# Optimization experiments

Measured on AMD Instinct MI355X. Metric: run time of the kernel, lower is better.

The kernel has to match this reference:

```python
import jax, jax.numpy as jnp
import numpy as np
import math

D_MODEL = 1024
NHEAD = 16
D_K = D_MODEL // NHEAD
LAMDA_ATT = 1.0
B, L = 2, 2048


def setup_inputs() -> dict:
    key = jax.random.key(0)
    ks = jax.random.split(key, 10)
    s = 1.0 / math.sqrt(D_MODEL)
    x = jax.random.normal(ks[0], (B, L, D_MODEL), dtype=jnp.float32)
    delta_r = jax.random.uniform(ks[1], (B, L), dtype=jnp.float32)  # positive, fed to log
    Wq = jax.random.normal(ks[2], (D_MODEL, D_MODEL), dtype=jnp.float32) * s
    Wk = jax.random.normal(ks[3], (D_MODEL, D_MODEL), dtype=jnp.float32) * s
    Wv = jax.random.normal(ks[4], (D_MODEL, D_MODEL), dtype=jnp.float32) * s
    Wo = jax.random.normal(ks[5], (D_MODEL, D_MODEL), dtype=jnp.float32) * s
    bq = jnp.zeros((D_MODEL,), jnp.float32)
    bk = jnp.zeros((D_MODEL,), jnp.float32)
    bv = jnp.zeros((D_MODEL,), jnp.float32)
    bo = jnp.zeros((D_MODEL,), jnp.float32)
    return {"x": x, "delta_r": delta_r, "Wq": Wq, "bq": bq, "Wk": Wk, "bk": bk,
            "Wv": Wv, "bv": bv, "Wo": Wo, "bo": bo}


def reference(x, delta_r, Wq, bq, Wk, bk, Wv, bv, Wo, bo):
    b, l, d = x.shape
    h, dk = NHEAD, D_K

    def proj(y, W, bias):
        # [B,L,D] -> [B,H,L,dk]
        return (y @ W + bias).reshape(b, l, h, dk).transpose(0, 2, 1, 3)

    v_scaled = x * delta_r[..., None]
    q = proj(x, Wq, bq)
    k = proj(x, Wk, bk)
    v = proj(v_scaled, Wv, bv)

    scores = jnp.einsum('bhqd,bhkd->bhqk', q, k) / math.sqrt(dk)
    pos = jnp.arange(l)
    dist = jnp.abs(pos[None, :] - pos[:, None]).astype(scores.dtype)  # [L,L]
    rel_bias = LAMDA_ATT * jnp.log(delta_r + 1e-6)  # [B,L]
    scores = scores - dist[None, None] * 0.1 + rel_bias[:, None, None, :]

    attn = jax.nn.softmax(scores, axis=-1)  # dropout is identity in eval mode
    context = jnp.einsum('bhqk,bhkd->bqhd', attn, v).reshape(b, l, d)
    out = context @ Wo + bo
    return out, attn.mean(axis=1)
```

## Files before the change

kernel.cpp:

```cpp
#include <hip/hip_runtime.h>
#include <math.h>

#define DMODEL 1024
#define NHEAD  16
#define DK     64
#define BB     2
#define LL     2048
#define MTOT   (BB*LL)

#define LOG2E      1.4426950408889634f
#define SCQ        (0.125f * LOG2E)
#define C2LOG      (0.1f * LOG2E)
#define SKIP_BOUND (-24.0f)

typedef __bf16 bf16_t;
typedef __bf16 bf16x8 __attribute__((ext_vector_type(8)));
typedef __bf16 bf16x4 __attribute__((ext_vector_type(4)));
typedef float  f32x4  __attribute__((ext_vector_type(4)));

static __device__ __forceinline__ f32x4 mfma16(bf16x8 a, bf16x8 b, f32x4 c) {
    return __builtin_amdgcn_mfma_f32_16x16x32_bf16(a, b, c, 0, 0, 0);
}
static __device__ __forceinline__ float exp2f_fast(float x) {
    return __builtin_amdgcn_exp2f(x);
}
static __device__ __forceinline__ float log2f_fast(float x) {
    return __builtin_amdgcn_logf(x);
}
static __device__ __forceinline__ void gl_lds16(const bf16_t* g, bf16_t* l) {
    __builtin_amdgcn_global_load_lds(
        (const __attribute__((address_space(1))) unsigned int*)g,
        (__attribute__((address_space(3))) unsigned int*)l, 16, 0, 0);
}

__global__ __launch_bounds__(256) void prep_x_k(
    const float* __restrict__ x, const float* __restrict__ dr,
    bf16_t* __restrict__ xb, float* __restrict__ logd2)
{
    size_t gid = (size_t)blockIdx.x * 256 + threadIdx.x;
    size_t off = gid * 8;
    float4 a = *(const float4*)(x + off);
    float4 c = *(const float4*)(x + off + 4);
    float va[8] = {a.x, a.y, a.z, a.w, c.x, c.y, c.z, c.w};
    bf16x8 o1;
#pragma unroll
    for (int j = 0; j < 8; ++j) o1[j] = (bf16_t)va[j];
    *(bf16x8*)(xb + off) = o1;
    if (gid < MTOT) logd2[gid] = log2f_fast(dr[gid] + 1e-6f);
}

__global__ __launch_bounds__(256) void prep_w_k(
    const float* __restrict__ Wq, const float* __restrict__ Wk,
    const float* __restrict__ Wv, const float* __restrict__ Wo,
    bf16_t* __restrict__ Wcat, bf16_t* __restrict__ Wot)
{
    __shared__ __align__(16) float Ts[64][68];
    const int z = blockIdx.z;
    const float* W = (z == 0) ? Wq : (z == 1) ? Wk : (z == 2) ? Wv : Wo;
    bf16_t* dst = (z < 3) ? (Wcat + (size_t)z * DMODEL * DMODEL) : Wot;
    const int tid = threadIdx.x;
    const int k0 = blockIdx.x * 64, n0 = blockIdx.y * 64;
#pragma unroll
    for (int i = 0; i < 4; ++i) {
        int u = tid + 256 * i, r = u >> 4, c4 = (u & 15) * 4;
        *(float4*)&Ts[r][c4] = *(const float4*)(W + (size_t)(k0 + r) * DMODEL + n0 + c4);
    }
    __syncthreads();
#pragma unroll
    for (int i = 0; i < 2; ++i) {
        int u = tid + 256 * i, n = u >> 3, k8 = (u & 7) * 8;
        bf16x8 v;
#pragma unroll
        for (int j = 0; j < 8; ++j) v[j] = (bf16_t)Ts[k8 + j][n];
        *(bf16x8*)(dst + (size_t)(n0 + n) * DMODEL + k0 + k8) = v;
    }
}

__global__ __launch_bounds__(256, 3) void gemm128_k(
    const bf16_t* __restrict__ A, const bf16_t* __restrict__ Bt,
    const float* __restrict__ b0, const float* __restrict__ b1,
    const float* __restrict__ b2, const float* __restrict__ delta,
    float* __restrict__ outf, bf16_t* __restrict__ outQ,
    bf16_t* __restrict__ outK, bf16_t* __restrict__ outVt, int mode)
{
    __shared__ __align__(16) bf16_t Asw[128 * 64];
    __shared__ __align__(16) bf16_t Bsw[128 * 64];
    const int tid = threadIdx.x, lane = tid & 63, w = tid >> 6;
    const int quad = lane >> 4, n16 = lane & 15;
    const int wm = (w & 1) * 64, wn = (w >> 1) * 64;
    const int m0 = blockIdx.y * 128, n0 = blockIdx.x * 128;
    const int srow = lane >> 3;
    const int scb  = (lane & 7) ^ srow;

    f32x4 acc[4][4] = {};

    for (int K0 = 0; K0 < DMODEL; K0 += 64) {
        __syncthreads();
#pragma unroll
        for (int i = 0; i < 4; ++i) {
            int rb = w * 32 + i * 8;
            gl_lds16(A  + (size_t)(m0 + rb + srow) * DMODEL + K0 + scb * 8,
                     &Asw[rb * 64]);
            gl_lds16(Bt + (size_t)(n0 + rb + srow) * DMODEL + K0 + scb * 8,
                     &Bsw[rb * 64]);
        }
        __syncthreads();
#pragma unroll
        for (int kc = 0; kc < 2; ++kc) {
            const int pcb = ((kc * 4 + quad) ^ (n16 & 7)) * 8;
            bf16x8 af[4], bfv[4];
#pragma unroll
            for (int mi = 0; mi < 4; ++mi)
                af[mi] = *(const bf16x8*)&Asw[(wm + mi * 16 + n16) * 64 + pcb];
#pragma unroll
            for (int ni = 0; ni < 4; ++ni)
                bfv[ni] = *(const bf16x8*)&Bsw[(wn + ni * 16 + n16) * 64 + pcb];
#pragma unroll
            for (int mi = 0; mi < 4; ++mi)
#pragma unroll
                for (int ni = 0; ni < 4; ++ni)
                    acc[mi][ni] = mfma16(af[mi], bfv[ni], acc[mi][ni]);
        }
    }

    if (mode == 0) {
        const int region = n0 >> 10;
        if (region == 2) {
#pragma unroll
            for (int mi = 0; mi < 4; ++mi) {
                const int mbase = m0 + wm + mi * 16 + quad * 4;
                const int bidx = mbase >> 11, l = mbase & (LL - 1);
                const f32x4 dm4 = *(const f32x4*)(delta + mbase);
#pragma unroll
                for (int ni = 0; ni < 4; ++ni) {
                    const int nl = (n0 & 1023) + wn + ni * 16 + n16;
                    const int h = nl >> 6, dd = nl & 63;
                    const float bv = b2[nl];
                    bf16x4 pk;
#pragma unroll
                    for (int r = 0; r < 4; ++r)
                        pk[r] = (bf16_t)(acc[mi][ni][r] * dm4[r] + bv);
                    *(bf16x4*)(outVt + ((size_t)(bidx * NHEAD + h) * DK + dd) * LL + l) = pk;
                }
            }
        } else {
            const float* bias = (region == 0) ? b0 : b1;
            bf16_t* dst = (region == 0) ? outQ : outK;
            const float qs = (region == 0) ? SCQ : 1.0f;
#pragma unroll
            for (int mi = 0; mi < 4; ++mi) {
#pragma unroll
                for (int r = 0; r < 4; ++r) {
                    const int m = m0 + wm + mi * 16 + quad * 4 + r;
                    const int bidx = m >> 11, l = m & (LL - 1);
#pragma unroll
                    for (int ni = 0; ni < 4; ++ni) {
                        const int nl = (n0 & 1023) + wn + ni * 16 + n16;
                        const int h = nl >> 6, dd = nl & 63;
                        float v = (acc[mi][ni][r] + bias[nl]) * qs;
                        dst[(((size_t)(bidx * NHEAD + h) * LL) + l) * DK + dd] = (bf16_t)v;
                    }
                }
            }
        }
    } else {
#pragma unroll
        for (int mi = 0; mi < 4; ++mi) {
#pragma unroll
            for (int r = 0; r < 4; ++r) {
                const int m = m0 + wm + mi * 16 + quad * 4 + r;
#pragma unroll
                for (int ni = 0; ni < 4; ++ni) {
                    const int n = n0 + wn + ni * 16 + n16;
                    outf[(size_t)m * DMODEL + n] = acc[mi][ni][r] + b0[n];
                }
            }
        }
    }
}

__global__ __launch_bounds__(256, 4) void gemm_out_k(
    const bf16_t* __restrict__ A, const bf16_t* __restrict__ Bt,
    const float* __restrict__ b0, float* __restrict__ outf)
{
    __shared__ __align__(16) bf16_t Asw[64 * 64];
    __shared__ __align__(16) bf16_t Bsw[128 * 64];
    const int tid = threadIdx.x, lane = tid & 63, w = tid >> 6;
    const int quad = lane >> 4, n16 = lane & 15;
    const int wm = (w & 1) * 32, wn = (w >> 1) * 64;
    const int m0 = blockIdx.y * 64, n0 = blockIdx.x * 128;
    const int srow = lane >> 3;
    const int scb  = (lane & 7) ^ srow;

    f32x4 acc[2][4] = {};

    for (int K0 = 0; K0 < DMODEL; K0 += 64) {
        __syncthreads();
#pragma unroll
        for (int i = 0; i < 2; ++i) {
            int rb = w * 16 + i * 8;
            gl_lds16(A + (size_t)(m0 + rb + srow) * DMODEL + K0 + scb * 8,
                     &Asw[rb * 64]);
        }
#pragma unroll
        for (int i = 0; i < 4; ++i) {
            int rb = w * 32 + i * 8;
            gl_lds16(Bt + (size_t)(n0 + rb + srow) * DMODEL + K0 + scb * 8,
                     &Bsw[rb * 64]);
        }
        __syncthreads();
#pragma unroll
        for (int kc = 0; kc < 2; ++kc) {
            const int pcb = ((kc * 4 + quad) ^ (n16 & 7)) * 8;
            bf16x8 af[2], bfv[4];
#pragma unroll
            for (int mi = 0; mi < 2; ++mi)
                af[mi] = *(const bf16x8*)&Asw[(wm + mi * 16 + n16) * 64 + pcb];
#pragma unroll
            for (int ni = 0; ni < 4; ++ni)
                bfv[ni] = *(const bf16x8*)&Bsw[(wn + ni * 16 + n16) * 64 + pcb];
#pragma unroll
            for (int mi = 0; mi < 2; ++mi)
#pragma unroll
                for (int ni = 0; ni < 4; ++ni)
                    acc[mi][ni] = mfma16(af[mi], bfv[ni], acc[mi][ni]);
        }
    }
#pragma unroll
    for (int mi = 0; mi < 2; ++mi) {
#pragma unroll
        for (int r = 0; r < 4; ++r) {
            const int m = m0 + wm + mi * 16 + quad * 4 + r;
#pragma unroll
            for (int ni = 0; ni < 4; ++ni) {
                const int n = n0 + wn + ni * 16 + n16;
                outf[(size_t)m * DMODEL + n] = acc[mi][ni][r] + b0[n];
            }
        }
    }
}

__global__ __launch_bounds__(256) void stats_k(
    const bf16_t* __restrict__ Q, const bf16_t* __restrict__ K,
    const float* __restrict__ logd2, float* __restrict__ Qn,
    float* __restrict__ Kn, float* __restrict__ dlb, float* __restrict__ ldx)
{
    __shared__ float qn_s[2048], kn_s[2048], dg_s[2048];
    const int tid = threadIdx.x, bh = blockIdx.x, b = bh >> 4;
    const size_t base = (size_t)bh * LL * DK;
#pragma unroll
    for (int i = 0; i < 8; ++i) {
        const int row = tid + 256 * i;
        float qn2 = 0.f, kn2 = 0.f, dg = 0.f;
#pragma unroll
        for (int j = 0; j < 8; ++j) {
            bf16x8 qv = *(const bf16x8*)(Q + base + (size_t)row * DK + j * 8);
            bf16x8 kv = *(const bf16x8*)(K + base + (size_t)row * DK + j * 8);
#pragma unroll
            for (int e = 0; e < 8; ++e) {
                float fq = (float)qv[e], fk = (float)kv[e];
                qn2 += fq * fq; kn2 += fk * fk; dg += fq * fk;
            }
        }
        qn_s[row] = qn2;
        kn_s[row] = kn2;
        dg_s[row] = dg + logd2[b * LL + row];
    }
    __syncthreads();
    if (tid < 16) {
        float mq = 0.f, md = 1e30f;
        for (int r = 0; r < 128; ++r) {
            mq = fmaxf(mq, qn_s[tid * 128 + r]);
            md = fminf(md, dg_s[tid * 128 + r]);
        }
        Qn[bh * 16 + tid] = sqrtf(mq);
        dlb[bh * 16 + tid] = md;
    } else if (tid >= 64 && tid < 96) {
        const int t = tid - 64;
        float mk = 0.f;
        for (int r = 0; r < 64; ++r) mk = fmaxf(mk, kn_s[t * 64 + r]);
        Kn[bh * 32 + t] = sqrtf(mk);
    } else if (tid >= 128 && tid < 160 && (bh & 15) == 0) {
        const int t = tid - 128;
        float ml = -1e30f;
        for (int r = 0; r < 64; ++r) ml = fmaxf(ml, logd2[b * LL + t * 64 + r]);
        ldx[b * 32 + t] = ml;
    }
}

__global__ __launch_bounds__(256) void mlstat_k(
    const float* __restrict__ mlws, float* __restrict__ mlmin)
{
    __shared__ float s[2048];
    const int tid = threadIdx.x, bh = blockIdx.x;
#pragma unroll
    for (int i = 0; i < 8; ++i)
        s[tid + 256 * i] = mlws[(size_t)bh * LL + tid + 256 * i];
    __syncthreads();
    if (tid < 16) {
        float m = 1e30f;
        for (int r = 0; r < 128; ++r) m = fminf(m, s[tid * 128 + r]);
        mlmin[bh * 16 + tid] = m;
    }
}

__global__ __launch_bounds__(256, 4) void attn_flash_mfma_k(
    const bf16_t* __restrict__ Q, const bf16_t* __restrict__ K,
    const bf16_t* __restrict__ Vt, const float* __restrict__ logd2,
    const float* __restrict__ Qn, const float* __restrict__ Kn,
    const float* __restrict__ dlb, const float* __restrict__ ldx,
    bf16_t* __restrict__ ctx, float* __restrict__ mlout)
{
    __shared__ __align__(16) bf16_t Ks[64][72];
    __shared__ __align__(16) bf16_t Vts[64][72];
    __shared__ __align__(16) bf16_t Ps[4][16][72];
    __shared__ float logds[64];

    const int tid = threadIdx.x;
    const int lane = tid & 63, w = tid >> 6;
    const int quad = lane >> 4, n16 = lane & 15;
    const int bh = blockIdx.x, b = bh >> 4, h = bh & 15;
    const int qt = blockIdx.y, q0 = qt * 64;
    const size_t base = (size_t)bh * LL * DK;
    const int q = q0 + w * 16 + n16;

    bf16x8 qa[2];
#pragma unroll
    for (int kc = 0; kc < 2; ++kc)
        qa[kc] = *(const bf16x8*)(Q + base + (size_t)q * DK + kc * 32 + quad * 8);

    unsigned mask = 0;
    {
        const float qn = Qn[bh * 16 + (qt >> 1)], dl = dlb[bh * 16 + (qt >> 1)];
        for (int t = 0; t < 32; ++t) {
            const int kc0 = t * 64;
            const int dmin = (kc0 > q0 + 63) ? (kc0 - (q0 + 63))
                           : ((q0 > kc0 + 63) ? (q0 - (kc0 + 63)) : 0);
            const float bound = qn * Kn[bh * 32 + t] + ldx[b * 32 + t]
                              - C2LOG * (float)dmin - dl;
            if (bound > SKIP_BOUND) mask |= (1u << t);
        }
    }

    const int strow = tid >> 3, stc8 = (tid & 7) * 8;
    bf16x8 kr0, kr1, vr0, vr1;
    float ldr = 0.f;
    auto prefetch = [&](int k0) {
        kr0 = *(const bf16x8*)(K + base + (size_t)(k0 + strow) * DK + stc8);
        kr1 = *(const bf16x8*)(K + base + (size_t)(k0 + 32 + strow) * DK + stc8);
        vr0 = *(const bf16x8*)(Vt + base + (size_t)strow * LL + k0 + stc8);
        vr1 = *(const bf16x8*)(Vt + base + (size_t)(32 + strow) * LL + k0 + stc8);
        if (tid < 64) ldr = logd2[b * LL + k0 + tid];
    };

    float m_c = -1e30f, l_c = 0.f;
    f32x4 o[4] = {};
    const float dfq = (float)(q - quad * 4);

    int t = (int)__builtin_ctz(mask);
    prefetch(t * 64);
    for (;;) {
        const unsigned rem = (t < 31) ? (mask >> (t + 1)) : 0u;
        const int tn = rem ? (t + 1 + (int)__builtin_ctz(rem)) : -1;
        __syncthreads();
        *(bf16x8*)&Ks[strow][stc8]       = kr0;
        *(bf16x8*)&Ks[32 + strow][stc8]  = kr1;
        *(bf16x8*)&Vts[strow][stc8]      = vr0;
        *(bf16x8*)&Vts[32 + strow][stc8] = vr1;
        if (tid < 64) logds[tid] = ldr;
        __syncthreads();
        if (tn >= 0) prefetch(tn * 64);
        const int k0 = t * 64;

        f32x4 s[4] = {};
#pragma unroll
        for (int kc = 0; kc < 2; ++kc) {
#pragma unroll
            for (int kt = 0; kt < 4; ++kt) {
                bf16x8 kb = *(const bf16x8*)&Ks[kt * 16 + n16][kc * 32 + quad * 8];
                s[kt] = mfma16(kb, qa[kc], s[kt]);
            }
        }
        const float df = dfq - (float)k0;
#pragma unroll
        for (int kt = 0; kt < 4; ++kt) {
            f32x4 ldv = *(const f32x4*)&logds[kt * 16 + quad * 4];
#pragma unroll
            for (int r = 0; r < 4; ++r)
                s[kt][r] += ldv[r] - C2LOG * fabsf(df - (float)(kt * 16 + r));
        }
        f32x4 mx;
#pragma unroll
        for (int r = 0; r < 4; ++r)
            mx[r] = fmaxf(fmaxf(s[0][r], s[1][r]), fmaxf(s[2][r], s[3][r]));
        float rm = fmaxf(fmaxf(mx[0], mx[1]), fmaxf(mx[2], mx[3]));
        rm = fmaxf(rm, __shfl_xor(rm, 16));
        rm = fmaxf(rm, __shfl_xor(rm, 32));
        const float mn = fmaxf(m_c, rm);
        const float alpha = exp2f_fast(m_c - mn);
        if (__any(mn > m_c)) {
#pragma unroll
            for (int dt = 0; dt < 4; ++dt)
#pragma unroll
                for (int r = 0; r < 4; ++r) o[dt][r] *= alpha;
        }
        f32x4 ps = {0.f, 0.f, 0.f, 0.f};
#pragma unroll
        for (int kt = 0; kt < 4; ++kt)
#pragma unroll
            for (int r = 0; r < 4; ++r) {
                float p = exp2f_fast(s[kt][r] - mn);
                s[kt][r] = p;
                ps[r] += p;
            }
        float psum = (ps[0] + ps[1]) + (ps[2] + ps[3]);
        psum += __shfl_xor(psum, 16);
        psum += __shfl_xor(psum, 32);
        l_c = l_c * alpha + psum;
        m_c = mn;
#pragma unroll
        for (int kt = 0; kt < 4; ++kt) {
            bf16x4 pk;
#pragma unroll
            for (int r = 0; r < 4; ++r) pk[r] = (bf16_t)s[kt][r];
            *(bf16x4*)&Ps[w][n16][kt * 16 + quad * 4] = pk;
        }
        __threadfence_block();
#pragma unroll
        for (int kc = 0; kc < 2; ++kc) {
            bf16x8 pa = *(const bf16x8*)&Ps[w][n16][kc * 32 + quad * 8];
#pragma unroll
            for (int dt = 0; dt < 4; ++dt) {
                bf16x8 vb = *(const bf16x8*)&Vts[dt * 16 + n16][kc * 32 + quad * 8];
                o[dt] = mfma16(vb, pa, o[dt]);
            }
        }
        if (tn < 0) break;
        t = tn;
    }
    const float inv = 1.f / l_c;
#pragma unroll
    for (int dt = 0; dt < 4; ++dt) {
        bf16x4 ov;
#pragma unroll
        for (int r = 0; r < 4; ++r) ov[r] = (bf16_t)(o[dt][r] * inv);
        *(bf16x4*)(ctx + ((size_t)b * LL + q) * DMODEL + h * DK +
                   dt * 16 + quad * 4) = ov;
    }
    if (quad == 0)
        mlout[(size_t)bh * LL + q] = m_c + log2f_fast(l_c);
}

__global__ __launch_bounds__(256, 3) void attn_mean_mfma_k(
    const bf16_t* __restrict__ Q, const bf16_t* __restrict__ K,
    const float* __restrict__ logd2, const float* __restrict__ mlws,
    const float* __restrict__ Qn, const float* __restrict__ Kn,
    const float* __restrict__ mlmin, const float* __restrict__ ldx,
    float* __restrict__ outmean)
{
    __shared__ __align__(16) bf16_t Ks[2][64][72];
    __shared__ float mls[2][128];
    __shared__ float logds[64];

    const int tid = threadIdx.x;
    const int lane = tid & 63, w = tid >> 6;
    const int quad = lane >> 4, n16 = lane & 15;
    const int k0 = blockIdx.x * 64, q0 = blockIdx.y * 128, b = blockIdx.z;
    const int qq[2] = {q0 + w * 32 + n16, q0 + w * 32 + 16 + n16};

    if (tid < 64) logds[tid] = logd2[b * LL + k0 + tid];
    __syncthreads();

    float bias0[2][4][4];
#pragma unroll
    for (int qg = 0; qg < 2; ++qg) {
        const float df = (float)(qq[qg] - k0 - quad * 4);
#pragma unroll
        for (int kt = 0; kt < 4; ++kt) {
            f32x4 ldv = *(const f32x4*)&logds[kt * 16 + quad * 4];
#pragma unroll
            for (int r = 0; r < 4; ++r)
                bias0[qg][kt][r] = ldv[r] - C2LOG * fabsf(df - (float)(kt * 16 + r));
        }
    }

    const int qt = q0 >> 7, ktl = k0 >> 6;
    const int dmin = (k0 > q0 + 127) ? (k0 - (q0 + 127))
                   : ((q0 > k0 + 63) ? (q0 - (k0 + 63)) : 0);
    unsigned hmask = 0;
    {
        const float dterm = ldx[b * 32 + ktl] - C2LOG * (float)dmin;
        for (int h = 0; h < NHEAD; ++h) {
            const int bh = b * 16 + h;
            const float bound = Qn[bh * 16 + qt] * Kn[bh * 32 + ktl] + dterm
                              - mlmin[bh * 16 + qt];
            if (bound > SKIP_BOUND) hmask |= (1u << h);
        }
    }

    f32x4 acc[2][4] = {};

    if (hmask) {
        const int strow = tid >> 3, stc8 = (tid & 7) * 8;
        bf16x8 kr0, kr1, qan[2][2];
        float mlv = 0.f;
        auto load_head = [&](int h) {
            const size_t hb = (size_t)(b * NHEAD + h) * LL * DK;
            kr0 = *(const bf16x8*)(K + hb + (size_t)(k0 + strow) * DK + stc8);
            kr1 = *(const bf16x8*)(K + hb + (size_t)(k0 + 32 + strow) * DK + stc8);
#pragma unroll
            for (int qg = 0; qg < 2; ++qg)
#pragma unroll
                for (int kc = 0; kc < 2; ++kc)
                    qan[qg][kc] = *(const bf16x8*)(Q + hb + (size_t)qq[qg] * DK +
                                                   kc * 32 + quad * 8);
            if (tid < 128) mlv = mlws[(size_t)(b * NHEAD + h) * LL + q0 + tid];
        };

        int h = (int)__builtin_ctz(hmask);
        load_head(h);
        int pc = 0;
        for (;;) {
            const unsigned rem = (h < 15) ? (hmask >> (h + 1)) : 0u;
            const int hn = rem ? (h + 1 + (int)__builtin_ctz(rem)) : -1;
            const int p = pc & 1;
            *(bf16x8*)&Ks[p][strow][stc8]      = kr0;
            *(bf16x8*)&Ks[p][32 + strow][stc8] = kr1;
            if (tid < 128) mls[p][tid] = mlv;
            bf16x8 qc[2][2] = {{qan[0][0], qan[0][1]}, {qan[1][0], qan[1][1]}};
            __syncthreads();
            if (hn >= 0) load_head(hn);

            f32x4 s[2][4] = {};
#pragma unroll
            for (int kc = 0; kc < 2; ++kc) {
#pragma unroll
                for (int kt = 0; kt < 4; ++kt) {
                    bf16x8 kb = *(const bf16x8*)&Ks[p][kt * 16 + n16][kc * 32 + quad * 8];
                    s[0][kt] = mfma16(kb, qc[0][kc], s[0][kt]);
                    s[1][kt] = mfma16(kb, qc[1][kc], s[1][kt]);
                }
            }
#pragma unroll
            for (int qg = 0; qg < 2; ++qg) {
                const float ml = mls[p][w * 32 + qg * 16 + n16];
#pragma unroll
                for (int kt = 0; kt < 4; ++kt)
#pragma unroll
                    for (int r = 0; r < 4; ++r)
                        acc[qg][kt][r] += exp2f_fast(s[qg][kt][r] +
                                                     bias0[qg][kt][r] - ml);
            }
            ++pc;
            if (hn < 0) break;
            h = hn;
        }
    }

    const float invH = 1.f / (float)NHEAD;
#pragma unroll
    for (int qg = 0; qg < 2; ++qg)
#pragma unroll
        for (int kt = 0; kt < 4; ++kt) {
            f32x4 ov;
#pragma unroll
            for (int r = 0; r < 4; ++r) ov[r] = acc[qg][kt][r] * invH;
            *(f32x4*)(outmean + ((size_t)b * LL + qq[qg]) * LL + k0 +
                      kt * 16 + quad * 4) = ov;
        }
}

extern "C" void kernel_launch(void* const* d_in, const int* in_sizes, int n_in,
                              void* d_out, int out_size, void* d_ws, size_t ws_size,
                              hipStream_t stream) {
    const float* x  = (const float*)d_in[0];
    const float* dr = (const float*)d_in[1];
    const float* Wq = (const float*)d_in[2];
    const float* bq = (const float*)d_in[3];
    const float* Wk = (const float*)d_in[4];
    const float* bk = (const float*)d_in[5];
    const float* Wv = (const float*)d_in[6];
    const float* bv = (const float*)d_in[7];
    const float* Wo = (const float*)d_in[8];
    const float* bo = (const float*)d_in[9];
    float* out = (float*)d_out;
    char* ws = (char*)d_ws;
    const size_t MB = 1ull << 20;

    bf16_t* xb   = (bf16_t*)(ws);
    bf16_t* Wcat = (bf16_t*)(ws + 8 * MB);
    bf16_t* Wot  = (bf16_t*)(ws + 14 * MB);
    bf16_t* Qb   = (bf16_t*)(ws + 16 * MB);
    bf16_t* Kb   = (bf16_t*)(ws + 24 * MB);
    bf16_t* Vtb  = (bf16_t*)(ws + 32 * MB);
    float*  logd = (float*)(ws + 40 * MB);
    float*  mlws = (float*)(ws + 41 * MB);
    float*  Qns  = (float*)(ws + 42 * MB);
    float*  Kns  = (float*)(ws + 42 * MB + 4096);
    float*  dlb  = (float*)(ws + 42 * MB + 12288);
    float*  ldxp = (float*)(ws + 42 * MB + 16384);
    float*  mlmn = (float*)(ws + 42 * MB + 20480);
    bf16_t* ctx  = xb;

    prep_x_k<<<2048, 256, 0, stream>>>(x, dr, xb, logd);
    prep_w_k<<<dim3(16, 16, 4), 256, 0, stream>>>(Wq, Wk, Wv, Wo, Wcat, Wot);

    gemm128_k<<<dim3(24, 32), 256, 0, stream>>>(xb, Wcat, bq, bk, bv, dr,
                                                nullptr, Qb, Kb, Vtb, 0);
    stats_k<<<32, 256, 0, stream>>>(Qb, Kb, logd, Qns, Kns, dlb, ldxp);

    attn_flash_mfma_k<<<dim3(32, 32), 256, 0, stream>>>(Qb, Kb, Vtb, logd,
                                                        Qns, Kns, dlb, ldxp,
                                                        ctx, mlws);
    mlstat_k<<<32, 256, 0, stream>>>(mlws, mlmn);
    attn_mean_mfma_k<<<dim3(32, 16, 2), 256, 0, stream>>>(
        Qb, Kb, logd, mlws, Qns, Kns, mlmn, ldxp,
        out + (size_t)MTOT * DMODEL);
    gemm_out_k<<<dim3(8, 64), 256, 0, stream>>>(ctx, Wot, bo, out);
}
```

Before: 240.1 us.

## Rewrite QKV projection GEMM as 256x256 tile with double-buffered phased pipeline

Replaces the 128x128, 4-wave QKV GEMM with a 256x256 tile using 8 waves. Global-to-LDS loads are double-buffered and split across four compute phases so the next K-slice loads while MFMAs run, with explicit vmcnt waits, barriers and s_setprio around the MFMA bursts. The larger tile raises data reuse per LDS load and removes the unused fp32 output mode. The price is 128KB of LDS per block and only 192 blocks, which may underfill the GPU's CUs and leave tail imbalance.

```diff
diff --git a/kernel.cpp b/kernel.cpp
--- a/kernel.cpp
+++ b/kernel.cpp
@@ -76,103 +76,143 @@
     }
 }
 
-__global__ __launch_bounds__(256, 3) void gemm128_k(
+__global__ __launch_bounds__(512, 2) void gemm256_qkv_k(
     const bf16_t* __restrict__ A, const bf16_t* __restrict__ Bt,
     const float* __restrict__ b0, const float* __restrict__ b1,
     const float* __restrict__ b2, const float* __restrict__ delta,
-    float* __restrict__ outf, bf16_t* __restrict__ outQ,
-    bf16_t* __restrict__ outK, bf16_t* __restrict__ outVt, int mode)
-{
-    __shared__ __align__(16) bf16_t Asw[128 * 64];
-    __shared__ __align__(16) bf16_t Bsw[128 * 64];
+    bf16_t* __restrict__ outQ, bf16_t* __restrict__ outK,
+    bf16_t* __restrict__ outVt)
+{
+    __shared__ __align__(16) bf16_t As[2][256 * 64];
+    __shared__ __align__(16) bf16_t Bs[2][256 * 64];
     const int tid = threadIdx.x, lane = tid & 63, w = tid >> 6;
     const int quad = lane >> 4, n16 = lane & 15;
-    const int wm = (w & 1) * 64, wn = (w >> 1) * 64;
-    const int m0 = blockIdx.y * 128, n0 = blockIdx.x * 128;
+    const int wr = w >> 2, wc = w & 3;
+    const int m0 = blockIdx.y * 256, n0 = blockIdx.x * 256;
     const int srow = lane >> 3;
     const int scb  = (lane & 7) ^ srow;
 
-    f32x4 acc[4][4] = {};
-
-    for (int K0 = 0; K0 < DMODEL; K0 += 64) {
-        __syncthreads();
-#pragma unroll
-        for (int i = 0; i < 4; ++i) {
-            int rb = w * 32 + i * 8;
-            gl_lds16(A  + (size_t)(m0 + rb + srow) * DMODEL + K0 + scb * 8,
-                     &Asw[rb * 64]);
-            gl_lds16(Bt + (size_t)(n0 + rb + srow) * DMODEL + K0 + scb * 8,
-                     &Bsw[rb * 64]);
-        }
-        __syncthreads();
-#pragma unroll
-        for (int kc = 0; kc < 2; ++kc) {
-            const int pcb = ((kc * 4 + quad) ^ (n16 & 7)) * 8;
-            bf16x8 af[4], bfv[4];
-#pragma unroll
-            for (int mi = 0; mi < 4; ++mi)
-                af[mi] = *(const bf16x8*)&Asw[(wm + mi * 16 + n16) * 64 + pcb];
-#pragma unroll
-            for (int ni = 0; ni < 4; ++ni)
-                bfv[ni] = *(const bf16x8*)&Bsw[(wn + ni * 16 + n16) * 64 + pcb];
-#pragma unroll
-            for (int mi = 0; mi < 4; ++mi)
-#pragma unroll
-                for (int ni = 0; ni < 4; ++ni)
-                    acc[mi][ni] = mfma16(af[mi], bfv[ni], acc[mi][ni]);
-        }
-    }
-
-    if (mode == 0) {
-        const int region = n0 >> 10;
-        if (region == 2) {
-#pragma unroll
-            for (int mi = 0; mi < 4; ++mi) {
-                const int mbase = m0 + wm + mi * 16 + quad * 4;
-                const int bidx = mbase >> 11, l = mbase & (LL - 1);
-                const f32x4 dm4 = *(const f32x4*)(delta + mbase);
+    f32x4 acc[8][4] = {};
+
+    auto stageA = [&](int h, int sp, int K0t) {
+#pragma unroll
+        for (int i = 0; i < 2; ++i) {
+            const int rloc = (w >> 2) * 128 + (w & 3) * 16 + h * 64 + i * 8;
+            gl_lds16(A + (size_t)(m0 + rloc + srow) * DMODEL + K0t + scb * 8,
+                     &As[sp][rloc * 64]);
+        }
+    };
+    auto stageB = [&](int h, int sp, int K0t) {
+#pragma unroll
+        for (int i = 0; i < 2; ++i) {
+            const int rloc = (w >> 1) * 64 + (w & 1) * 16 + h * 32 + i * 8;
+            gl_lds16(Bt + (size_t)(n0 + rloc + srow) * DMODEL + K0t + scb * 8,
+                     &Bs[sp][rloc * 64]);
+        }
+    };
+
+#define PHASE(QM, QN, PBUF, STA, STH, STP, STK, STPRED, WVM)                    \
+    do {                                                                        \
+        bf16x8 af0[4], af1[4], bv0[2], bv1[2];                                  \
+        {                                                                       \
+            const int pcb0 = ((0 * 4 + quad) ^ (n16 & 7)) * 8;                  \
+            const int pcb1 = ((1 * 4 + quad) ^ (n16 & 7)) * 8;                  \
+            _Pragma("unroll")                                                   \
+            for (int mi = 0; mi < 4; ++mi) {                                    \
+                const int ra = (wr * 128 + (QM) * 64 + mi * 16 + n16) * 64;     \
+                af0[mi] = *(const bf16x8*)&As[PBUF][ra + pcb0];                 \
+                af1[mi] = *(const bf16x8*)&As[PBUF][ra + pcb1];                 \
+            }                                                                   \
+            _Pragma("unroll")                                                   \
+            for (int ni = 0; ni < 2; ++ni) {                                    \
+                const int rb = (wc * 64 + (QN) * 32 + ni * 16 + n16) * 64;      \
+                bv0[ni] = *(const bf16x8*)&Bs[PBUF][rb + pcb0];                 \
+                bv1[ni] = *(const bf16x8*)&Bs[PBUF][rb + pcb1];                 \
+            }                                                                   \
+        }                                                                       \
+        if (STPRED) { if (STA) stageA(STH, STP, STK); else stageB(STH, STP, STK); } \
+        __builtin_amdgcn_s_barrier();                                           \
+        asm volatile("s_waitcnt lgkmcnt(0)" ::: "memory");                      \
+        __builtin_amdgcn_s_setprio(1);                                          \
+        _Pragma("unroll")                                                       \
+        for (int mi = 0; mi < 4; ++mi)                                          \
+            _Pragma("unroll")                                                   \
+            for (int ni = 0; ni < 2; ++ni)                                      \
+                acc[(QM) * 4 + mi][(QN) * 2 + ni] =                             \
+                    mfma16(af0[mi], bv0[ni], acc[(QM) * 4 + mi][(QN) * 2 + ni]);\
+        _Pragma("unroll")                                                       \
+        for (int mi = 0; mi < 4; ++mi)                                          \
+            _Pragma("unroll")                                                   \
+            for (int ni = 0; ni < 2; ++ni)                                      \
+                acc[(QM) * 4 + mi][(QN) * 2 + ni] =                             \
+                    mfma16(af1[mi], bv1[ni], acc[(QM) * 4 + mi][(QN) * 2 + ni]);\
+        __builtin_amdgcn_s_setprio(0);                                          \
+        if ((WVM) == 6) asm volatile("s_waitcnt vmcnt(6)" ::: "memory");        \
+        if ((WVM) == 8) asm volatile("s_waitcnt vmcnt(8)" ::: "memory");        \
+        __builtin_amdgcn_s_barrier();                                           \
+    } while (0)
+
+    stageA(0, 0, 0);
+    stageB(0, 0, 0);
+    stageA(1, 0, 0);
+    stageB(1, 0, 0);
+    stageA(0, 1, 64);
+    stageB(0, 1, 64);
+    asm volatile("s_waitcnt vmcnt(4)" ::: "memory");
+    __builtin_amdgcn_s_barrier();
+
+    for (int u = 0; u < 15; ++u) {
+        const int p = u & 1;
+        const bool st2 = (u < 14);
+        const int K1 = (u + 1) * 64, K2 = (u + 2) * 64;
+        PHASE(0, 0, p, true,  1, 1 - p, K1, true, 6);
+        PHASE(0, 1, p, false, 1, 1 - p, K1, true, -1);
+        PHASE(1, 0, p, true,  0, p,     K2, st2, -1);
+        PHASE(1, 1, p, false, 0, p,     K2, st2, 8);
+    }
+    asm volatile("s_waitcnt vmcnt(0)" ::: "memory");
+    __builtin_amdgcn_s_barrier();
+    PHASE(0, 0, 1, false, 0, 0, 0, false, -1);
+    PHASE(0, 1, 1, false, 0, 0, 0, false, -1);
+    PHASE(1, 0, 1, false, 0, 0, 0, false, -1);
+    PHASE(1, 1, 1, false, 0, 0, 0, false, -1);
+#undef PHASE
+
+    const int region = n0 >> 10;
+    if (region == 2) {
+#pragma unroll
+        for (int mi = 0; mi < 8; ++mi) {
+            const int mbase = m0 + wr * 128 + mi * 16 + quad * 4;
+            const int bidx = mbase >> 11, l = mbase & (LL - 1);
+            const f32x4 dm4 = *(const f32x4*)(delta + mbase);
+#pragma unroll
+            for (int ni = 0; ni < 4; ++ni) {
+                const int nl = (n0 & 1023) + wc * 64 + ni * 16 + n16;
+                const int h = nl >> 6, dd = nl & 63;
+                const float bv = b2[nl];
+                bf16x4 pk;
+#pragma unroll
+                for (int r = 0; r < 4; ++r)
+                    pk[r] = (bf16_t)(acc[mi][ni][r] * dm4[r] + bv);
+                *(bf16x4*)(outVt + ((size_t)(bidx * NHEAD + h) * DK + dd) * LL + l) = pk;
+            }
+        }
+    } else {
+        const float* bias = (region == 0) ? b0 : b1;
+        bf16_t* dst = (region == 0) ? outQ : outK;
+        const float qs = (region == 0) ? SCQ : 1.0f;
+#pragma unroll
+        for (int mi = 0; mi < 8; ++mi) {
+#pragma unroll
+            for (int r = 0; r < 4; ++r) {
+                const int m = m0 + wr * 128 + mi * 16 + quad * 4 + r;
+                const int bidx = m >> 11, l = m & (LL - 1);
 #pragma unroll
                 for (int ni = 0; ni < 4; ++ni) {
-                    const int nl = (n0 & 1023) + wn + ni * 16 + n16;
+                    const int nl = (n0 & 1023) + wc * 64 + ni * 16 + n16;
                     const int h = nl >> 6, dd = nl & 63;
-                    const float bv = b2[nl];
-                    bf16x4 pk;
-#pragma unroll
-                    for (int r = 0; r < 4; ++r)
-                        pk[r] = (bf16_t)(acc[mi][ni][r] * dm4[r] + bv);
-                    *(bf16x4*)(outVt + ((size_t)(bidx * NHEAD + h) * DK + dd) * LL + l) = pk;
-                }
-            }
-        } else {
-            const float* bias = (region == 0) ? b0 : b1;
-            bf16_t* dst = (region == 0) ? outQ : outK;
-            const float qs = (region == 0) ? SCQ : 1.0f;
-#pragma unroll
-            for (int mi = 0; mi < 4; ++mi) {
-#pragma unroll
-                for (int r = 0; r < 4; ++r) {
-                    const int m = m0 + wm + mi * 16 + quad * 4 + r;
-                    const int bidx = m >> 11, l = m & (LL - 1);
-#pragma unroll
-                    for (int ni = 0; ni < 4; ++ni) {
-                        const int nl = (n0 & 1023) + wn + ni * 16 + n16;
-                        const int h = nl >> 6, dd = nl & 63;
-                        float v = (acc[mi][ni][r] + bias[nl]) * qs;
-                        dst[(((size_t)(bidx * NHEAD + h) * LL) + l) * DK + dd] = (bf16_t)v;
-                    }
-                }
-            }
-        }
-    } else {
-#pragma unroll
-        for (int mi = 0; mi < 4; ++mi) {
-#pragma unroll
-            for (int r = 0; r < 4; ++r) {
-                const int m = m0 + wm + mi * 16 + quad * 4 + r;
-#pragma unroll
-                for (int ni = 0; ni < 4; ++ni) {
-                    const int n = n0 + wn + ni * 16 + n16;
-                    outf[(size_t)m * DMODEL + n] = acc[mi][ni][r] + b0[n];
+                    float v = (acc[mi][ni][r] + bias[nl]) * qs;
+                    dst[(((size_t)(bidx * NHEAD + h) * LL) + l) * DK + dd] = (bf16_t)v;
                 }
             }
         }
@@ -605,8 +645,8 @@
     prep_x_k<<<2048, 256, 0, stream>>>(x, dr, xb, logd);
     prep_w_k<<<dim3(16, 16, 4), 256, 0, stream>>>(Wq, Wk, Wv, Wo, Wcat, Wot);
 
-    gemm128_k<<<dim3(24, 32), 256, 0, stream>>>(xb, Wcat, bq, bk, bv, dr,
-                                                nullptr, Qb, Kb, Vtb, 0);
+    gemm256_qkv_k<<<dim3(12, 16), 512, 0, stream>>>(xb, Wcat, bq, bk, bv, dr,
+                                                    Qb, Kb, Vtb);
     stats_k<<<32, 256, 0, stream>>>(Qb, Kb, logd, Qns, Kns, dlb, ldxp);
 
     attn_flash_mfma_k<<<dim3(32, 32), 256, 0, stream>>>(Qb, Kb, Vtb, logd,
```

New measurement: 254.7 us. 1.06x slower.

## Merge prep kernels and fuse output GEMM with attention-mean kernel

Applied to the files above, without the earlier changes.

Combines the x-conversion and weight-transpose prep kernels into one launch with block-index dispatch. It also merges the output projection GEMM and the attention-mean kernel into a single launch, so the two independent tails can run concurrently on the GPU. The goal is to cut launch overhead and tail idle time. In exchange, the fused tail kernel reserves shared memory for both paths, which may reduce occupancy, and register pressure is set by the larger branch.

```diff
diff --git a/kernel.cpp b/kernel.cpp
--- a/kernel.cpp
+++ b/kernel.cpp
@@ -33,46 +33,47 @@
         (__attribute__((address_space(3))) unsigned int*)l, 16, 0, 0);
 }
 
-__global__ __launch_bounds__(256) void prep_x_k(
+__global__ __launch_bounds__(256) void prep_fused_k(
     const float* __restrict__ x, const float* __restrict__ dr,
-    bf16_t* __restrict__ xb, float* __restrict__ logd2)
-{
-    size_t gid = (size_t)blockIdx.x * 256 + threadIdx.x;
-    size_t off = gid * 8;
-    float4 a = *(const float4*)(x + off);
-    float4 c = *(const float4*)(x + off + 4);
-    float va[8] = {a.x, a.y, a.z, a.w, c.x, c.y, c.z, c.w};
-    bf16x8 o1;
-#pragma unroll
-    for (int j = 0; j < 8; ++j) o1[j] = (bf16_t)va[j];
-    *(bf16x8*)(xb + off) = o1;
-    if (gid < MTOT) logd2[gid] = log2f_fast(dr[gid] + 1e-6f);
-}
-
-__global__ __launch_bounds__(256) void prep_w_k(
+    bf16_t* __restrict__ xb, float* __restrict__ logd2,
     const float* __restrict__ Wq, const float* __restrict__ Wk,
     const float* __restrict__ Wv, const float* __restrict__ Wo,
     bf16_t* __restrict__ Wcat, bf16_t* __restrict__ Wot)
 {
     __shared__ __align__(16) float Ts[64][68];
-    const int z = blockIdx.z;
-    const float* W = (z == 0) ? Wq : (z == 1) ? Wk : (z == 2) ? Wv : Wo;
-    bf16_t* dst = (z < 3) ? (Wcat + (size_t)z * DMODEL * DMODEL) : Wot;
+    const int bid = blockIdx.x;
     const int tid = threadIdx.x;
-    const int k0 = blockIdx.x * 64, n0 = blockIdx.y * 64;
-#pragma unroll
-    for (int i = 0; i < 4; ++i) {
-        int u = tid + 256 * i, r = u >> 4, c4 = (u & 15) * 4;
-        *(float4*)&Ts[r][c4] = *(const float4*)(W + (size_t)(k0 + r) * DMODEL + n0 + c4);
-    }
-    __syncthreads();
-#pragma unroll
-    for (int i = 0; i < 2; ++i) {
-        int u = tid + 256 * i, n = u >> 3, k8 = (u & 7) * 8;
-        bf16x8 v;
-#pragma unroll
-        for (int j = 0; j < 8; ++j) v[j] = (bf16_t)Ts[k8 + j][n];
-        *(bf16x8*)(dst + (size_t)(n0 + n) * DMODEL + k0 + k8) = v;
+    if (bid < 2048) {
+        size_t gid = (size_t)bid * 256 + tid;
+        size_t off = gid * 8;
+        float4 a = *(const float4*)(x + off);
+        float4 c = *(const float4*)(x + off + 4);
+        float va[8] = {a.x, a.y, a.z, a.w, c.x, c.y, c.z, c.w};
+        bf16x8 o1;
+#pragma unroll
+        for (int j = 0; j < 8; ++j) o1[j] = (bf16_t)va[j];
+        *(bf16x8*)(xb + off) = o1;
+        if (gid < MTOT) logd2[gid] = log2f_fast(dr[gid] + 1e-6f);
+    } else {
+        const int t = bid - 2048;
+        const int z = t >> 8;
+        const float* W = (z == 0) ? Wq : (z == 1) ? Wk : (z == 2) ? Wv : Wo;
+        bf16_t* dst = (z < 3) ? (Wcat + (size_t)z * DMODEL * DMODEL) : Wot;
+        const int k0 = (t & 15) * 64, n0 = ((t >> 4) & 15) * 64;
+#pragma unroll
+        for (int i = 0; i < 4; ++i) {
+            int u = tid + 256 * i, r = u >> 4, c4 = (u & 15) * 4;
+            *(float4*)&Ts[r][c4] = *(const float4*)(W + (size_t)(k0 + r) * DMODEL + n0 + c4);
+        }
+        __syncthreads();
+#pragma unroll
+        for (int i = 0; i < 2; ++i) {
+            int u = tid + 256 * i, n = u >> 3, k8 = (u & 7) * 8;
+            bf16x8 v;
+#pragma unroll
+            for (int j = 0; j < 8; ++j) v[j] = (bf16_t)Ts[k8 + j][n];
+            *(bf16x8*)(dst + (size_t)(n0 + n) * DMODEL + k0 + k8) = v;
+        }
     }
 }
 
@@ -179,67 +180,6 @@
     }
 }
 
-__global__ __launch_bounds__(256, 4) void gemm_out_k(
-    const bf16_t* __restrict__ A, const bf16_t* __restrict__ Bt,
-    const float* __restrict__ b0, float* __restrict__ outf)
-{
-    __shared__ __align__(16) bf16_t Asw[64 * 64];
-    __shared__ __align__(16) bf16_t Bsw[128 * 64];
-    const int tid = threadIdx.x, lane = tid & 63, w = tid >> 6;
-    const int quad = lane >> 4, n16 = lane & 15;
-    const int wm = (w & 1) * 32, wn = (w >> 1) * 64;
-    const int m0 = blockIdx.y * 64, n0 = blockIdx.x * 128;
-    const int srow = lane >> 3;
-    const int scb  = (lane & 7) ^ srow;
-
-    f32x4 acc[2][4] = {};
-
-    for (int K0 = 0; K0 < DMODEL; K0 += 64) {
-        __syncthreads();
-#pragma unroll
-        for (int i = 0; i < 2; ++i) {
-            int rb = w * 16 + i * 8;
-            gl_lds16(A + (size_t)(m0 + rb + srow) * DMODEL + K0 + scb * 8,
-                     &Asw[rb * 64]);
-        }
-#pragma unroll
-        for (int i = 0; i < 4; ++i) {
-            int rb = w * 32 + i * 8;
-            gl_lds16(Bt + (size_t)(n0 + rb + srow) * DMODEL + K0 + scb * 8,
-                     &Bsw[rb * 64]);
-        }
-        __syncthreads();
-#pragma unroll
-        for (int kc = 0; kc < 2; ++kc) {
-            const int pcb = ((kc * 4 + quad) ^ (n16 & 7)) * 8;
-            bf16x8 af[2], bfv[4];
-#pragma unroll
-            for (int mi = 0; mi < 2; ++mi)
-                af[mi] = *(const bf16x8*)&Asw[(wm + mi * 16 + n16) * 64 + pcb];
-#pragma unroll
-            for (int ni = 0; ni < 4; ++ni)
-                bfv[ni] = *(const bf16x8*)&Bsw[(wn + ni * 16 + n16) * 64 + pcb];
-#pragma unroll
-            for (int mi = 0; mi < 2; ++mi)
-#pragma unroll
-                for (int ni = 0; ni < 4; ++ni)
-                    acc[mi][ni] = mfma16(af[mi], bfv[ni], acc[mi][ni]);
-        }
-    }
-#pragma unroll
-    for (int mi = 0; mi < 2; ++mi) {
-#pragma unroll
-        for (int r = 0; r < 4; ++r) {
-            const int m = m0 + wm + mi * 16 + quad * 4 + r;
-#pragma unroll
-            for (int ni = 0; ni < 4; ++ni) {
-                const int n = n0 + wn + ni * 16 + n16;
-                outf[(size_t)m * DMODEL + n] = acc[mi][ni][r] + b0[n];
-            }
-        }
-    }
-}
-
 __global__ __launch_bounds__(256) void stats_k(
     const bf16_t* __restrict__ Q, const bf16_t* __restrict__ K,
     const float* __restrict__ logd2, float* __restrict__ Qn,
@@ -451,21 +391,83 @@
         mlout[(size_t)bh * LL + q] = m_c + log2f_fast(l_c);
 }
 
-__global__ __launch_bounds__(256, 3) void attn_mean_mfma_k(
+__global__ __launch_bounds__(256, 3) void tail_fused_k(
+    const bf16_t* __restrict__ A, const bf16_t* __restrict__ Bt,
+    const float* __restrict__ b0, float* __restrict__ outf,
     const bf16_t* __restrict__ Q, const bf16_t* __restrict__ K,
     const float* __restrict__ logd2, const float* __restrict__ mlws,
     const float* __restrict__ Qn, const float* __restrict__ Kn,
     const float* __restrict__ mlmin, const float* __restrict__ ldx,
     float* __restrict__ outmean)
 {
+    __shared__ __align__(16) bf16_t Asw[64 * 64];
+    __shared__ __align__(16) bf16_t Bsw[128 * 64];
     __shared__ __align__(16) bf16_t Ks[2][64][72];
     __shared__ float mls[2][128];
     __shared__ float logds[64];
 
+    const int bid = blockIdx.x;
     const int tid = threadIdx.x;
     const int lane = tid & 63, w = tid >> 6;
     const int quad = lane >> 4, n16 = lane & 15;
-    const int k0 = blockIdx.x * 64, q0 = blockIdx.y * 128, b = blockIdx.z;
+
+    if (bid < 512) {
+        const int wm = (w & 1) * 32, wn = (w >> 1) * 64;
+        const int m0 = (bid >> 3) * 64, n0 = (bid & 7) * 128;
+        const int srow = lane >> 3;
+        const int scb  = (lane & 7) ^ srow;
+
+        f32x4 acc[2][4] = {};
+
+        for (int K0 = 0; K0 < DMODEL; K0 += 64) {
+            __syncthreads();
+#pragma unroll
+            for (int i = 0; i < 2; ++i) {
+                int rb = w * 16 + i * 8;
+                gl_lds16(A + (size_t)(m0 + rb + srow) * DMODEL + K0 + scb * 8,
+                         &Asw[rb * 64]);
+            }
+#pragma unroll
+            for (int i = 0; i < 4; ++i) {
+                int rb = w * 32 + i * 8;
+                gl_lds16(Bt + (size_t)(n0 + rb + srow) * DMODEL + K0 + scb * 8,
+                         &Bsw[rb * 64]);
+            }
+            __syncthreads();
+#pragma unroll
+            for (int kc = 0; kc < 2; ++kc) {
+                const int pcb = ((kc * 4 + quad) ^ (n16 & 7)) * 8;
+                bf16x8 af[2], bfv[4];
+#pragma unroll
+                for (int mi = 0; mi < 2; ++mi)
+                    af[mi] = *(const bf16x8*)&Asw[(wm + mi * 16 + n16) * 64 + pcb];
+#pragma unroll
+                for (int ni = 0; ni < 4; ++ni)
+                    bfv[ni] = *(const bf16x8*)&Bsw[(wn + ni * 16 + n16) * 64 + pcb];
+#pragma unroll
+                for (int mi = 0; mi < 2; ++mi)
+#pragma unroll
+                    for (int ni = 0; ni < 4; ++ni)
+                        acc[mi][ni] = mfma16(af[mi], bfv[ni], acc[mi][ni]);
+            }
+        }
+#pragma unroll
+        for (int mi = 0; mi < 2; ++mi) {
+#pragma unroll
+            for (int r = 0; r < 4; ++r) {
+                const int m = m0 + wm + mi * 16 + quad * 4 + r;
+#pragma unroll
+                for (int ni = 0; ni < 4; ++ni) {
+                    const int n = n0 + wn + ni * 16 + n16;
+                    outf[(size_t)m * DMODEL + n] = acc[mi][ni][r] + b0[n];
+                }
+            }
+        }
+        return;
+    }
+
+    const int tb = bid - 512;
+    const int k0 = (tb & 31) * 64, q0 = ((tb >> 5) & 15) * 128, b = tb >> 9;
     const int qq[2] = {q0 + w * 32 + n16, q0 + w * 32 + 16 + n16};
 
     if (tid < 64) logds[tid] = logd2[b * LL + k0 + tid];
@@ -602,8 +604,8 @@
     float*  mlmn = (float*)(ws + 42 * MB + 20480);
     bf16_t* ctx  = xb;
 
-    prep_x_k<<<2048, 256, 0, stream>>>(x, dr, xb, logd);
-    prep_w_k<<<dim3(16, 16, 4), 256, 0, stream>>>(Wq, Wk, Wv, Wo, Wcat, Wot);
+    prep_fused_k<<<3072, 256, 0, stream>>>(x, dr, xb, logd,
+                                           Wq, Wk, Wv, Wo, Wcat, Wot);
 
     gemm128_k<<<dim3(24, 32), 256, 0, stream>>>(xb, Wcat, bq, bk, bv, dr,
                                                 nullptr, Qb, Kb, Vtb, 0);
@@ -613,8 +615,8 @@
                                                         Qns, Kns, dlb, ldxp,
                                                         ctx, mlws);
     mlstat_k<<<32, 256, 0, stream>>>(mlws, mlmn);
-    attn_mean_mfma_k<<<dim3(32, 16, 2), 256, 0, stream>>>(
-        Qb, Kb, logd, mlws, Qns, Kns, mlmn, ldxp,
-        out + (size_t)MTOT * DMODEL);
-    gemm_out_k<<<dim3(8, 64), 256, 0, stream>>>(ctx, Wot, bo, out);
-}
+    tail_fused_k<<<1536, 256, 0, stream>>>(ctx, Wot, bo, out,
+                                           Qb, Kb, logd, mlws, Qns, Kns,
+                                           mlmn, ldxp,
+                                           out + (size_t)MTOT * DMODEL);
+}
```

After: 238.0 us. About the same (-0.9%).
